# Optimization experiments

Hardware: AMD Instinct MI355X
Metric: run time of the kernel (lower is better)

## Reference

```python
import jax, jax.numpy as jnp
import numpy as np

H, D = 24, 128
HID = H * D  # 3072
IP_DIM = 2048
B, S_IMG, S_TXT, L_IP = 1, 1024, 512, 16
EPS = 1e-6
IP_SCALE = 1.0


def _rms(x, w):
    v = jnp.mean(jnp.square(x), axis=-1, keepdims=True)
    return x * jax.lax.rsqrt(v + EPS) * w


def _heads(x):
    b, s, _ = x.shape
    return x.reshape(b, s, H, D).transpose(0, 2, 1, 3)  # [b,H,s,D]


def _unheads(x):
    b, h, s, d = x.shape
    return x.transpose(0, 2, 1, 3).reshape(b, s, h * d)


def _rope(x, cos, sin):
    # diffusers flux apply_rotary_emb (use_real, unbind_dim=-1): interleaved pairs
    xr = x.reshape(x.shape[:-1] + (D // 2, 2))
    xrot = jnp.stack([-xr[..., 1], xr[..., 0]], axis=-1).reshape(x.shape)
    return x * cos + xrot * sin


def _sdpa(q, k, v):
    scale = 1.0 / jnp.sqrt(jnp.asarray(D, q.dtype))
    s = jnp.einsum('bhqd,bhkd->bhqk', q, k) * scale
    return jnp.einsum('bhqk,bhkd->bhqd', jax.nn.softmax(s, axis=-1), v)


def setup_inputs() -> dict:
    ks = iter(jax.random.split(jax.random.key(0), 24))
    std = 0.02
    lin = lambda k, di, do: std * jax.random.normal(k, (di, do), jnp.float32)
    z = lambda: jnp.zeros((HID,), jnp.float32)
    ones = lambda: jnp.ones((D,), jnp.float32)
    return {
        'hidden_states': jax.random.normal(next(ks), (B, S_IMG, HID), jnp.float32),
        'encoder_hidden_states': jax.random.normal(next(ks), (B, S_TXT, HID), jnp.float32),
        'ip_hidden_states': jax.random.normal(next(ks), (B, L_IP, IP_DIM), jnp.float32),
        'rope_cos': jax.random.uniform(next(ks), (S_TXT + S_IMG, D), jnp.float32),
        'rope_sin': jax.random.uniform(next(ks), (S_TXT + S_IMG, D), jnp.float32),
        'Wq': lin(next(ks), HID, HID), 'bq': z(),
        'Wk': lin(next(ks), HID, HID), 'bk': z(),
        'Wv': lin(next(ks), HID, HID), 'bv': z(),
        'norm_q_w': ones(), 'norm_k_w': ones(),
        'Waq': lin(next(ks), HID, HID), 'baq': z(),
        'Wak': lin(next(ks), HID, HID), 'bak': z(),
        'Wav': lin(next(ks), HID, HID), 'bav': z(),
        'norm_added_q_w': ones(), 'norm_added_k_w': ones(),
        'Wo': lin(next(ks), HID, HID), 'bo': z(),
        'Wadd_out': lin(next(ks), HID, HID), 'badd_out': z(),
        'Wk_ip': lin(next(ks), IP_DIM, HID), 'bk_ip': z(),
        'Wv_ip': lin(next(ks), IP_DIM, HID), 'bv_ip': z(),
        'norm_ip_q_w': ones(), 'norm_ip_k_w': ones(),
    }


def reference(hidden_states, encoder_hidden_states, ip_hidden_states, rope_cos, rope_sin,
              Wq, bq, Wk, bk, Wv, bv, norm_q_w, norm_k_w,
              Waq, baq, Wak, bak, Wav, bav, norm_added_q_w, norm_added_k_w,
              Wo, bo, Wadd_out, badd_out,
              Wk_ip, bk_ip, Wv_ip, bv_ip, norm_ip_q_w, norm_ip_k_w):
    s_txt = encoder_hidden_states.shape[1]
    # image-token projections
    q = hidden_states @ Wq + bq
    k = hidden_states @ Wk + bk
    v = hidden_states @ Wv + bv

    # IP-adapter cross-attention branch (uses q pre-RMSNorm / pre-RoPE)
    ip_q = _rms(_heads(q), norm_ip_q_w)                               # [B,H,S_img,D]
    ip_k = _rms(_heads(ip_hidden_states @ Wk_ip + bk_ip), norm_ip_k_w)  # [B,H,L_ip,D]
    ip_v = _heads(ip_hidden_states @ Wv_ip + bv_ip)
    ip_out = _unheads(_sdpa(ip_q, ip_k, ip_v))                        # [B,S_img,HID]

    qh = _rms(_heads(q), norm_q_w)
    kh = _rms(_heads(k), norm_k_w)
    vh = _heads(v)

    # text-token (encoder) projections
    eq = _rms(_heads(encoder_hidden_states @ Waq + baq), norm_added_q_w)
    ek = _rms(_heads(encoder_hidden_states @ Wak + bak), norm_added_k_w)
    ev = _heads(encoder_hidden_states @ Wav + bav)

    qf = _rope(jnp.concatenate([eq, qh], axis=2), rope_cos, rope_sin)
    kf = _rope(jnp.concatenate([ek, kh], axis=2), rope_cos, rope_sin)
    vf = jnp.concatenate([ev, vh], axis=2)

    out = _unheads(_sdpa(qf, kf, vf))                                 # [B,S_txt+S_img,HID]
    enc_out, img_out = out[:, :s_txt], out[:, s_txt:]
    img_out = img_out + ip_out * IP_SCALE
    img_out = img_out @ Wo + bo
    enc_out = enc_out @ Wadd_out + badd_out
    return (img_out, enc_out)
```

## Files before the change

kernel.cpp:

```cpp
#include <hip/hip_runtime.h>

typedef __bf16 bf16x8 __attribute__((ext_vector_type(8)));
typedef float f32x4 __attribute__((ext_vector_type(4)));
typedef unsigned short u16;
typedef unsigned int u32;

#define QSCALE 0.08838834764831845f

static __device__ __forceinline__ float bf2f(u16 u) {
  union { float f; u32 i; } x; x.i = ((u32)u) << 16; return x.f;
}
static __device__ __forceinline__ u16 f2bf(float f) {
  union { float f; u32 i; } x; x.f = f;
  u32 r = x.i + 0x7fffu + ((x.i >> 16) & 1u);
  return (u16)(r >> 16);
}
static __device__ __forceinline__ void gload16(const void* gp, void* lp) {
  __builtin_amdgcn_global_load_lds(
      (const __attribute__((address_space(1))) u32*)gp,
      (__attribute__((address_space(3))) u32*)lp, 16, 0, 0);
}

__global__ __launch_bounds__(256) void k_conv_acts(
    const float* __restrict__ hs, const float* __restrict__ ehs, const float* __restrict__ iph,
    u16* __restrict__ hsb, u16* __restrict__ ehsb, u16* __restrict__ ipb)
{
  int i = blockIdx.x * 256 + threadIdx.x;
  const float* s; u16* d; int j;
  if (i < 786432)        { s = hs;  d = hsb;  j = i; }
  else if (i < 1179648)  { s = ehs; d = ehsb; j = i - 786432; }
  else                   { s = iph; d = ipb;  j = i - 1179648; }
  float4 v = ((const float4*)s)[j];
  uint2 o;
  o.x = (u32)f2bf(v.x) | ((u32)f2bf(v.y) << 16);
  o.y = (u32)f2bf(v.z) | ((u32)f2bf(v.w) << 16);
  ((uint2*)d)[j] = o;
}

struct WT { const float* src; u16* dst; int K; };
struct WTPack { WT w[10]; };

__global__ __launch_bounds__(256) void k_transp_w(WTPack p)
{
  WT d = p.w[blockIdx.z];
  int K = d.K;
  int k0 = blockIdx.y * 128;
  if (k0 >= K) return;
  int n0 = blockIdx.x * 128;
  __shared__ u32 T[128 * 64];
  int t = threadIdx.x;
  int lane = t & 63, w = t >> 6;
  const float* s = d.src + (size_t)(k0 + w * 32) * 3072 + n0 + lane * 2;
  float2 v[32];
  #pragma unroll
  for (int j = 0; j < 32; j++)
    v[j] = *(const float2*)(s + (size_t)j * 3072);
  int n = lane * 2;
  u32* r0 = T + (size_t)n * 64;
  u32* r1 = r0 + 64;
  int s0 = n & 31, s1 = (n + 1) & 31;
  #pragma unroll
  for (int pp = 0; pp < 16; pp++) {
    int c = w * 16 + pp;
    float2 a = v[2 * pp], b = v[2 * pp + 1];
    r0[c ^ s0] = (u32)f2bf(a.x) | ((u32)f2bf(b.x) << 16);
    r1[c ^ s1] = (u32)f2bf(a.y) | ((u32)f2bf(b.y) << 16);
  }
  __syncthreads();
  #pragma unroll
  for (int i = 0; i < 8; i++) {
    int idx = t + i * 256;
    int row = idx >> 4, ch = idx & 15;
    const u32* r2 = T + (size_t)row * 64;
    int sw = row & 31;
    uint4 o;
    o.x = r2[(ch * 4 + 0) ^ sw];
    o.y = r2[(ch * 4 + 1) ^ sw];
    o.z = r2[(ch * 4 + 2) ^ sw];
    o.w = r2[(ch * 4 + 3) ^ sw];
    *(uint4*)(d.dst + (size_t)(n0 + row) * K + k0 + ch * 8) = o;
  }
}

struct G8Job { const u16* A; const u16* W; const float* bias; void* C; int M; int K; int blk0; int out_f32; };
struct G8Pack { G8Job j[8]; int njobs; };

__global__ __launch_bounds__(512, 2) void k_gemm8(G8Pack p)
{
  extern __shared__ __align__(16) u16 smem[];
  u16* As = smem;
  u16* Bs = smem + 32768;

  int bid = blockIdx.x;
  bid = (bid & 7) * 30 + (bid >> 3);
  int ji = 0;
  while (ji + 1 < p.njobs && bid >= p.j[ji + 1].blk0) ji++;
  G8Job J = p.j[ji];
  int local = bid - J.blk0;
  int m0 = (local / 12) * 256;
  int n0 = (local % 12) * 256;
  int K = J.K, NT = K >> 6;

  int tid = threadIdx.x, w = tid >> 6, lane = tid & 63, l15 = lane & 15, quad = lane >> 4;
  int wm = (w >> 2) * 128, wn = (w & 3) * 64;
  int dw = w * 512;
  int cread = (quad ^ (l15 & 3)) * 8;

  int rr = tid >> 2;
  int c4 = ((tid & 3) ^ (rr & 3)) * 8;
  const u16* pa0 = J.A + (size_t)(m0 + rr) * K + c4;
  const u16* pa1 = pa0 + (size_t)128 * K;
  const u16* pb0 = J.W + (size_t)(n0 + rr) * K + c4;
  const u16* pb1 = pb0 + (size_t)128 * K;

  f32x4 acc[8][4] = {};
  bf16x8 af[4], bfr[4];

#define STAGE_A(b, kh, tt) do { int _ko = (tt) * 64 + (kh) * 32; int _d = ((b) * 2 + (kh)) * 8192 + dw; \
    gload16(pa0 + _ko, As + _d); gload16(pa1 + _ko, As + _d + 4096); } while (0)
#define STAGE_B(b, kh, tt) do { int _ko = (tt) * 64 + (kh) * 32; int _d = ((b) * 2 + (kh)) * 8192 + dw; \
    gload16(pb0 + _ko, Bs + _d); gload16(pb1 + _ko, Bs + _d + 4096); } while (0)

  STAGE_A(0, 0, 0); STAGE_B(0, 0, 0); STAGE_A(0, 1, 0); STAGE_B(0, 1, 0);
  STAGE_A(1, 0, 1); STAGE_B(1, 0, 1);
  __asm__ volatile("s_waitcnt vmcnt(4)" ::: "memory");
  __builtin_amdgcn_s_barrier();

#define PHASE(ks, mtb, READB, STAGES, WAITS) do { \
    int _ab = (cur * 2 + (ks)) * 8192; \
    _Pragma("unroll") for (int i = 0; i < 4; i++) \
      af[i] = *(const bf16x8*)(As + _ab + (wm + ((mtb) + i) * 16 + l15) * 32 + cread); \
    if (READB) { _Pragma("unroll") for (int i = 0; i < 4; i++) \
      bfr[i] = *(const bf16x8*)(Bs + _ab + (wn + i * 16 + l15) * 32 + cread); } \
    STAGES; WAITS; \
    __builtin_amdgcn_s_barrier(); \
    __asm__ volatile("s_waitcnt lgkmcnt(0)" ::: "memory"); \
    __builtin_amdgcn_sched_barrier(0); \
    __builtin_amdgcn_s_setprio(1); \
    _Pragma("unroll") for (int mt = 0; mt < 4; mt++) \
      _Pragma("unroll") for (int nt = 0; nt < 4; nt++) \
        acc[(mtb) + mt][nt] = __builtin_amdgcn_mfma_f32_16x16x32_bf16(af[mt], bfr[nt], acc[(mtb) + mt][nt], 0, 0, 0); \
    __builtin_amdgcn_s_setprio(0); \
    __builtin_amdgcn_sched_barrier(0); \
    __builtin_amdgcn_s_barrier(); \
  } while (0)

  int cur = 0;
  for (int t = 0; t < NT; t++) {
    int o = cur ^ 1;
    int t1 = (t + 1 < NT) ? t + 1 : NT - 1;
    int t2 = (t + 2 < NT) ? t + 2 : NT - 1;
    PHASE(0, 0, 1, STAGE_A(o, 1, t1), (void)0);
    PHASE(0, 4, 0, STAGE_B(o, 1, t1), __asm__ volatile("s_waitcnt vmcnt(8)" ::: "memory"));
    PHASE(1, 0, 1, STAGE_A(cur, 0, t2), (void)0);
    PHASE(1, 4, 0, STAGE_B(cur, 0, t2), __asm__ volatile("s_waitcnt vmcnt(8)" ::: "memory"));
    cur = o;
  }
  __asm__ volatile("s_waitcnt vmcnt(0)" ::: "memory");

  #pragma unroll
  for (int mt = 0; mt < 8; mt++) {
    int row = m0 + wm + mt * 16 + quad * 4;
    #pragma unroll
    for (int nt = 0; nt < 4; nt++) {
      int col = n0 + wn + nt * 16 + l15;
      float bv = J.bias[col];
      #pragma unroll
      for (int r = 0; r < 4; r++) {
        if (row + r < J.M) {
          float v = acc[mt][nt][r] + bv;
          if (J.out_f32) ((float*)J.C)[(size_t)(row + r) * 3072 + col] = v;
          else           ((u16*)J.C)[(size_t)(row + r) * 3072 + col] = f2bf(v);
        }
      }
    }
  }
#undef PHASE
#undef STAGE_A
#undef STAGE_B
}

struct GJob { const u16* A; const u16* W; const float* bias; void* C; int M; int K; int blk0; int out_f32; };
struct GPack { GJob j[8]; int njobs; };

template<int MT>
__global__ __launch_bounds__(256) void k_gemm(GPack p)
{
  __shared__ u16 As[MT * 64];
  __shared__ u16 Bs[128 * 64];
  int bid = blockIdx.x;
  int ji = 0;
  while (ji + 1 < p.njobs && bid >= p.j[ji+1].blk0) ji++;
  GJob J = p.j[ji];
  int local = bid - J.blk0;
  int m0 = (local / 24) * MT;
  int n0 = (local % 24) * 128;

  int tid = threadIdx.x, w = tid >> 6, lane = tid & 63, l15 = lane & 15, quad = lane >> 4;
  constexpr int MF = MT / 32;
  int wm = (w >> 1) * (MT / 2), wn = (w & 1) * 64;
  f32x4 acc[MF][4] = {};

  constexpr int GA = MT * 8 / 256;
  const u16* Ag[GA]; const u16* Bg[4];
  #pragma unroll
  for (int i = 0; i < GA; i++) {
    int s = i * 256 + tid;
    int row = s >> 3, kc = (s & 7) ^ (row & 7);
    Ag[i] = J.A + (size_t)(m0 + row) * J.K + kc * 8;
  }
  #pragma unroll
  for (int i = 0; i < 4; i++) {
    int s = i * 256 + tid;
    int row = s >> 3, kc = (s & 7) ^ (row & 7);
    Bg[i] = J.W + (size_t)(n0 + row) * J.K + kc * 8;
  }

  for (int k0 = 0; k0 < J.K; k0 += 64) {
    #pragma unroll
    for (int i = 0; i < GA; i++)
      gload16(Ag[i] + k0, As + (size_t)(i * 256 + w * 64) * 8);
    #pragma unroll
    for (int i = 0; i < 4; i++)
      gload16(Bg[i] + k0, Bs + (size_t)(i * 256 + w * 64) * 8);
    __syncthreads();
    int x7 = l15 & 7;
    #pragma unroll
    for (int ks = 0; ks < 2; ks++) {
      bf16x8 af[MF], bfr[4];
      #pragma unroll
      for (int t = 0; t < MF; t++)
        af[t] = *(const bf16x8*)(As + (wm + t * 16 + l15) * 64 + (((ks * 4 + quad) ^ x7) * 8));
      #pragma unroll
      for (int t = 0; t < 4; t++)
        bfr[t] = *(const bf16x8*)(Bs + (wn + t * 16 + l15) * 64 + (((ks * 4 + quad) ^ x7) * 8));
      #pragma unroll
      for (int mt = 0; mt < MF; mt++)
        #pragma unroll
        for (int nt = 0; nt < 4; nt++)
          acc[mt][nt] = __builtin_amdgcn_mfma_f32_16x16x32_bf16(af[mt], bfr[nt], acc[mt][nt], 0, 0, 0);
    }
    __syncthreads();
  }

  #pragma unroll
  for (int mt = 0; mt < MF; mt++) {
    int row = m0 + wm + mt * 16 + quad * 4;
    #pragma unroll
    for (int nt = 0; nt < 4; nt++) {
      int col = n0 + wn + nt * 16 + l15;
      float bv = J.bias[col];
      #pragma unroll
      for (int r = 0; r < 4; r++) {
        if (row + r < J.M) {
          float v = acc[mt][nt][r] + bv;
          if (J.out_f32) ((float*)J.C)[(size_t)(row + r) * 3072 + col] = v;
          else           ((u16*)J.C)[(size_t)(row + r) * 3072 + col] = f2bf(v);
        }
      }
    }
  }
}

__global__ __launch_bounds__(256) void k_pack_qk(
    const u16* __restrict__ q, const u16* __restrict__ k,
    const u16* __restrict__ eq, const u16* __restrict__ ek,
    const u16* __restrict__ ipk,
    const float* __restrict__ cosr, const float* __restrict__ sinr,
    const float* __restrict__ nq, const float* __restrict__ nk,
    const float* __restrict__ naq, const float* __restrict__ nak,
    const float* __restrict__ nipq, const float* __restrict__ nipk,
    u16* __restrict__ Qf, u16* __restrict__ Kf, u16* __restrict__ Qip, u16* __restrict__ Kip)
{
  int u = blockIdx.x * 4 + (threadIdx.x >> 6);
  int lane = threadIdx.x & 63;
  int d0 = lane * 2;
  if (u < 36864) {
    int t = u / 24, h = u % 24;
    bool txt = t < 512;
    const u16* qrow = txt ? eq + (size_t)t * 3072 : q + (size_t)(t - 512) * 3072;
    const u16* krow = txt ? ek + (size_t)t * 3072 : k + (size_t)(t - 512) * 3072;
    u32 qv = ((const u32*)(qrow + h * 128))[lane];
    u32 kv = ((const u32*)(krow + h * 128))[lane];
    float q0 = bf2f((u16)qv), q1 = bf2f((u16)(qv >> 16));
    float k0 = bf2f((u16)kv), k1 = bf2f((u16)(kv >> 16));
    float sq = q0 * q0 + q1 * q1, sk = k0 * k0 + k1 * k1;
    #pragma unroll
    for (int off = 32; off > 0; off >>= 1) {
      sq += __shfl_xor(sq, off, 64);
      sk += __shfl_xor(sk, off, 64);
    }
    float rq = rsqrtf(sq * (1.0f / 128.0f) + 1e-6f);
    float rk = rsqrtf(sk * (1.0f / 128.0f) + 1e-6f);
    const float* wq = txt ? naq : nq;
    const float* wk = txt ? nak : nk;
    float2 c = ((const float2*)(cosr + (size_t)t * 128))[lane];
    float2 s = ((const float2*)(sinr + (size_t)t * 128))[lane];
    float xq0 = q0 * rq * wq[d0] * QSCALE, xq1 = q1 * rq * wq[d0 + 1] * QSCALE;
    float xk0 = k0 * rk * wk[d0],          xk1 = k1 * rk * wk[d0 + 1];
    u32 oq = (u32)f2bf(xq0 * c.x - xq1 * s.x) | ((u32)f2bf(xq1 * c.y + xq0 * s.y) << 16);
    u32 ok = (u32)f2bf(xk0 * c.x - xk1 * s.x) | ((u32)f2bf(xk1 * c.y + xk0 * s.y) << 16);
    ((u32*)(Qf + ((size_t)h * 1536 + t) * 128))[lane] = oq;
    ((u32*)(Kf + ((size_t)h * 1536 + t) * 128))[lane] = ok;
    if (!txt) {
      float y0 = q0 * rq * nipq[d0] * QSCALE, y1 = q1 * rq * nipq[d0 + 1] * QSCALE;
      u32 oy = (u32)f2bf(y0) | ((u32)f2bf(y1) << 16);
      ((u32*)(Qip + ((size_t)h * 1024 + (t - 512)) * 128))[lane] = oy;
    }
  } else {
    int u2 = u - 36864;
    if (u2 < 384) {
      int h = u2 >> 4, t = u2 & 15;
      u32 v = ((const u32*)(ipk + (size_t)t * 3072 + h * 128))[lane];
      float x0 = bf2f((u16)v), x1 = bf2f((u16)(v >> 16));
      float ss = x0 * x0 + x1 * x1;
      #pragma unroll
      for (int off = 32; off > 0; off >>= 1) ss += __shfl_xor(ss, off, 64);
      float rr = rsqrtf(ss * (1.0f / 128.0f) + 1e-6f);
      u32 o = (u32)f2bf(x0 * rr * nipk[d0]) | ((u32)f2bf(x1 * rr * nipk[d0 + 1]) << 16);
      ((u32*)(Kip + ((size_t)h * 64 + t) * 128))[lane] = o;
    }
  }
}

__global__ __launch_bounds__(256) void k_pack_v(
    const u16* __restrict__ v, const u16* __restrict__ ev, const u16* __restrict__ ipv,
    u16* __restrict__ Vt, u16* __restrict__ Vipt)
{
  __shared__ u16 T[64 * 72];
  int h = blockIdx.x, y = blockIdx.y, tid = threadIdx.x;
  if (y < 48) {
    int tb = (y % 24) * 64, db = (y / 24) * 64;
    #pragma unroll
    for (int i = 0; i < 2; i++) {
      int idx = tid + i * 256;
      int r = idx >> 3, ch = idx & 7;
      int t = tb + r;
      const u16* src = (t < 512) ? ev + (size_t)t * 3072 : v + (size_t)(t - 512) * 3072;
      uint4 val = *(const uint4*)(src + h * 128 + db + ch * 8);
      u16 tmp[8];
      *(uint4*)tmp = val;
      #pragma unroll
      for (int j = 0; j < 8; j++) T[(ch * 8 + j) * 72 + r] = tmp[j];
    }
    __syncthreads();
    #pragma unroll
    for (int i = 0; i < 2; i++) {
      int idx = tid + i * 256;
      int r = idx >> 3, ch = idx & 7;
      uint4 val = *(const uint4*)(T + r * 72 + ch * 8);
      *(uint4*)(Vt + ((size_t)h * 128 + db + r) * 1536 + tb + ch * 8) = val;
    }
  } else {
    if (tid < 128) {
      #pragma unroll
      for (int t = 0; t < 64; t++) {
        u16 val = 0;
        if (t < 16) val = ipv[(size_t)t * 3072 + h * 128 + tid];
        Vipt[((size_t)h * 128 + tid) * 64 + t] = val;
      }
    }
  }
}

__global__ __launch_bounds__(256) void k_attn(
    const u16* __restrict__ Q, const u16* __restrict__ K, const u16* __restrict__ V,
    const float* __restrict__ addend, void* __restrict__ out,
    int Sq, int Skv, int Skv_valid, int mode)
{
  __shared__ u16 Ks[64 * 128];
  __shared__ u16 Vs[128 * 64];
  __shared__ u16 Ps[4 * 16 * 68];
  int tid = threadIdx.x, h = blockIdx.y;
  int w = tid >> 6, lane = tid & 63, l15 = lane & 15, quad = lane >> 4;
  int mb = blockIdx.x * 64 + w * 16;

  bf16x8 aq[4];
  {
    const u16* qp = Q + ((size_t)h * Sq + mb + l15) * 128 + quad * 8;
    #pragma unroll
    for (int c = 0; c < 4; c++) aq[c] = *(const bf16x8*)(qp + c * 32);
  }

  const u16* Kg[4]; const u16* Vg[4];
  #pragma unroll
  for (int i = 0; i < 4; i++) {
    int s = tid + i * 256;
    int key = s >> 4, kc = (s & 15) ^ (key & 15);
    Kg[i] = K + ((size_t)h * Skv + key) * 128 + kc * 8;
    int d = s >> 3, vc = (s & 7) ^ (d & 7);
    Vg[i] = V + ((size_t)h * 128 + d) * Skv + vc * 8;
  }

  f32x4 o[8] = {};
  float m_col = -3.0e38f, l_col = 0.0f;
  u16* myPs = Ps + w * (16 * 68);

  for (int kb = 0; kb < Skv; kb += 64) {
    #pragma unroll
    for (int i = 0; i < 4; i++) {
      gload16(Kg[i] + (size_t)kb * 128, Ks + (i * 256 + w * 64) * 8);
      gload16(Vg[i] + kb,               Vs + (i * 256 + w * 64) * 8);
    }
    __syncthreads();

    f32x4 sc[4];
    #pragma unroll
    for (int mt = 0; mt < 4; mt++) {
      f32x4 a = {0.f, 0.f, 0.f, 0.f};
      int key = mt * 16 + l15;
      #pragma unroll
      for (int c = 0; c < 4; c++) {
        bf16x8 kf = *(const bf16x8*)(Ks + key * 128 + (((c * 4 + quad) ^ l15) * 8));
        a = __builtin_amdgcn_mfma_f32_16x16x32_bf16(kf, aq[c], a, 0, 0, 0);
      }
      sc[mt] = a;
    }
    if (Skv_valid != Skv) {
      #pragma unroll
      for (int mt = 0; mt < 4; mt++)
        #pragma unroll
        for (int r = 0; r < 4; r++)
          if (kb + mt * 16 + quad * 4 + r >= Skv_valid) sc[mt][r] = -1e30f;
    }

    float mx = sc[0][0];
    #pragma unroll
    for (int mt = 0; mt < 4; mt++)
      #pragma unroll
      for (int r = 0; r < 4; r++) mx = fmaxf(mx, sc[mt][r]);
    mx = fmaxf(mx, __shfl_xor(mx, 16, 64));
    mx = fmaxf(mx, __shfl_xor(mx, 32, 64));
    float mn = fmaxf(m_col, mx);
    float alpha = __expf(m_col - mn);
    m_col = mn;

    float sum = 0.f;
    #pragma unroll
    for (int mt = 0; mt < 4; mt++) {
      u16 pk[4];
      #pragma unroll
      for (int r = 0; r < 4; r++) {
        float pp = __expf(sc[mt][r] - mn);
        sum += pp;
        pk[r] = f2bf(pp);
      }
      uint2 pv;
      pv.x = (u32)pk[0] | ((u32)pk[1] << 16);
      pv.y = (u32)pk[2] | ((u32)pk[3] << 16);
      *(uint2*)(myPs + l15 * 68 + mt * 16 + quad * 4) = pv;
    }
    sum += __shfl_xor(sum, 16, 64);
    sum += __shfl_xor(sum, 32, 64);
    l_col = l_col * alpha + sum;

    float ar[4];
    #pragma unroll
    for (int r = 0; r < 4; r++) ar[r] = __shfl(alpha, quad * 4 + r, 64);
    #pragma unroll
    for (int nt = 0; nt < 8; nt++) {
      o[nt][0] *= ar[0]; o[nt][1] *= ar[1]; o[nt][2] *= ar[2]; o[nt][3] *= ar[3];
    }

    __asm__ volatile("s_waitcnt lgkmcnt(0)" ::: "memory");
    #pragma unroll
    for (int kc = 0; kc < 2; kc++) {
      bf16x8 pa = *(const bf16x8*)(myPs + l15 * 68 + kc * 32 + quad * 8);
      #pragma unroll
      for (int nt = 0; nt < 8; nt++) {
        int d = nt * 16 + l15;
        bf16x8 vf = *(const bf16x8*)(Vs + d * 64 + (((kc * 4 + quad) ^ (d & 7)) * 8));
        o[nt] = __builtin_amdgcn_mfma_f32_16x16x32_bf16(pa, vf, o[nt], 0, 0, 0);
      }
    }
    __syncthreads();
  }

  float linv = 1.0f / l_col;
  float lr[4];
  #pragma unroll
  for (int r = 0; r < 4; r++) lr[r] = __shfl(linv, quad * 4 + r, 64);
  #pragma unroll
  for (int r = 0; r < 4; r++) {
    int t = mb + quad * 4 + r;
    size_t base = (size_t)t * 3072 + h * 128 + l15;
    if (mode == 0) {
      float* O = (float*)out;
      #pragma unroll
      for (int nt = 0; nt < 8; nt++) O[base + nt * 16] = o[nt][r] * lr[r];
    } else {
      u16* O = (u16*)out;
      #pragma unroll
      for (int nt = 0; nt < 8; nt++) {
        float vv = o[nt][r] * lr[r];
        if (t >= 512) vv += addend[(size_t)(t - 512) * 3072 + h * 128 + nt * 16 + l15];
        O[base + nt * 16] = f2bf(vv);
      }
    }
  }
}

extern "C" void kernel_launch(void* const* d_in, const int* in_sizes, int n_in,
                              void* d_out, int out_size, void* d_ws, size_t ws_size,
                              hipStream_t stream) {
  const float* hs   = (const float*)d_in[0];
  const float* ehs  = (const float*)d_in[1];
  const float* iph  = (const float*)d_in[2];
  const float* cosr = (const float*)d_in[3];
  const float* sinr = (const float*)d_in[4];
  const float* Wq   = (const float*)d_in[5];  const float* bq   = (const float*)d_in[6];
  const float* Wk   = (const float*)d_in[7];  const float* bk   = (const float*)d_in[8];
  const float* Wv   = (const float*)d_in[9];  const float* bv   = (const float*)d_in[10];
  const float* nq   = (const float*)d_in[11]; const float* nk   = (const float*)d_in[12];
  const float* Waq  = (const float*)d_in[13]; const float* baq  = (const float*)d_in[14];
  const float* Wak  = (const float*)d_in[15]; const float* bak  = (const float*)d_in[16];
  const float* Wav  = (const float*)d_in[17]; const float* bav  = (const float*)d_in[18];
  const float* naq  = (const float*)d_in[19]; const float* nak  = (const float*)d_in[20];
  const float* Wo   = (const float*)d_in[21]; const float* bo   = (const float*)d_in[22];
  const float* Wad  = (const float*)d_in[23]; const float* bad  = (const float*)d_in[24];
  const float* Wkip = (const float*)d_in[25]; const float* bkip = (const float*)d_in[26];
  const float* Wvip = (const float*)d_in[27]; const float* bvip = (const float*)d_in[28];
  const float* nipq = (const float*)d_in[29]; const float* nipk = (const float*)d_in[30];
  (void)in_sizes; (void)n_in; (void)out_size; (void)ws_size;

  char* ws = (char*)d_ws;
  size_t off = 0;
  auto alloc = [&](size_t bytes) { size_t o = off; off += (bytes + 255) & ~(size_t)255; return o; };

  u16* hsb  = (u16*)(ws + alloc((size_t)1024 * 3072 * 2));
  u16* ehsb = (u16*)(ws + alloc((size_t)512 * 3072 * 2));
  u16* ipb  = (u16*)(ws + alloc((size_t)16 * 2048 * 2));
  u16* WT_[10];
  for (int i = 0; i < 10; i++) WT_[i] = (u16*)(ws + alloc((size_t)3072 * (i < 8 ? 3072 : 2048) * 2));
  u16* qb   = (u16*)(ws + alloc((size_t)1024 * 3072 * 2));
  u16* kb_  = (u16*)(ws + alloc((size_t)1024 * 3072 * 2));
  u16* vb   = (u16*)(ws + alloc((size_t)1024 * 3072 * 2));
  u16* eqb  = (u16*)(ws + alloc((size_t)512 * 3072 * 2));
  u16* ekb  = (u16*)(ws + alloc((size_t)512 * 3072 * 2));
  u16* evb  = (u16*)(ws + alloc((size_t)512 * 3072 * 2));
  u16* ipkb = (u16*)(ws + alloc((size_t)16 * 3072 * 2));
  u16* ipvb = (u16*)(ws + alloc((size_t)16 * 3072 * 2));
  u16* Qf   = (u16*)(ws + alloc((size_t)24 * 1536 * 128 * 2));
  u16* Kff  = (u16*)(ws + alloc((size_t)24 * 1536 * 128 * 2));
  u16* Vt   = (u16*)(ws + alloc((size_t)24 * 128 * 1536 * 2));
  u16* Qip  = (u16*)(ws + alloc((size_t)24 * 1024 * 128 * 2));
  u16* Kip  = (u16*)(ws + alloc((size_t)24 * 64 * 128 * 2));
  u16* Vipt = (u16*)(ws + alloc((size_t)24 * 128 * 64 * 2));
  float* ip_out = (float*)(ws + alloc((size_t)1024 * 3072 * 4));
  u16* attnb = (u16*)(ws + alloc((size_t)1536 * 3072 * 2));

  static bool attr_done = false;
  if (!attr_done) {
    hipFuncSetAttribute((const void*)k_gemm8, hipFuncAttributeMaxDynamicSharedMemorySize, 131072);
    attr_done = true;
  }

  k_conv_acts<<<4640, 256, 0, stream>>>(hs, ehs, iph, hsb, ehsb, ipb);

  WTPack p;
  const float* wsrc[10] = {Wq, Wk, Wv, Waq, Wak, Wav, Wo, Wad, Wkip, Wvip};
  for (int i = 0; i < 10; i++) { p.w[i].src = wsrc[i]; p.w[i].dst = WT_[i]; p.w[i].K = (i < 8 ? 3072 : 2048); }
  k_transp_w<<<dim3(24, 24, 10), 256, 0, stream>>>(p);

  {
    G8Pack pp;
    const u16* As_[8]  = {hsb, hsb, hsb, ehsb, ehsb, ehsb, ipb, ipb};
    const u16* Ws_[8]  = {WT_[0], WT_[1], WT_[2], WT_[3], WT_[4], WT_[5], WT_[8], WT_[9]};
    const float* bs_[8] = {bq, bk, bv, baq, bak, bav, bkip, bvip};
    u16* Cs_[8]        = {qb, kb_, vb, eqb, ekb, evb, ipkb, ipvb};
    int Ms_[8] = {1024, 1024, 1024, 512, 512, 512, 16, 16};
    int Ks_[8] = {3072, 3072, 3072, 3072, 3072, 3072, 2048, 2048};
    int blk = 0;
    for (int i = 0; i < 8; i++) {
      pp.j[i].A = As_[i]; pp.j[i].W = Ws_[i]; pp.j[i].bias = bs_[i]; pp.j[i].C = Cs_[i];
      pp.j[i].M = Ms_[i]; pp.j[i].K = Ks_[i]; pp.j[i].blk0 = blk; pp.j[i].out_f32 = 0;
      blk += ((Ms_[i] + 255) / 256) * 12;
    }
    pp.njobs = 8;
    k_gemm8<<<dim3(blk), 512, 131072, stream>>>(pp);
  }

  k_pack_qk<<<9312, 256, 0, stream>>>(qb, kb_, eqb, ekb, ipkb, cosr, sinr, nq, nk, naq, nak, nipq, nipk, Qf, Kff, Qip, Kip);
  k_pack_v<<<dim3(24, 49), 256, 0, stream>>>(vb, evb, ipvb, Vt, Vipt);

  k_attn<<<dim3(16, 24), 256, 0, stream>>>(Qip, Kip, Vipt, (const float*)nullptr, ip_out, 1024, 64, 16, 0);
  k_attn<<<dim3(24, 24), 256, 0, stream>>>(Qf, Kff, Vt, ip_out, attnb, 1536, 1536, 1536, 1);

  {
    GPack pp;
    float* out = (float*)d_out;
    pp.j[0].A = attnb + (size_t)512 * 3072; pp.j[0].W = WT_[6]; pp.j[0].bias = bo;
    pp.j[0].C = out; pp.j[0].M = 1024; pp.j[0].K = 3072; pp.j[0].blk0 = 0; pp.j[0].out_f32 = 1;
    pp.j[1].A = attnb; pp.j[1].W = WT_[7]; pp.j[1].bias = bad;
    pp.j[1].C = out + (size_t)1024 * 3072; pp.j[1].M = 512; pp.j[1].K = 3072;
    pp.j[1].blk0 = (1024 / 64) * 24; pp.j[1].out_f32 = 1;
    pp.njobs = 2;
    k_gemm<64><<<dim3((1024 / 64) * 24 + (512 / 64) * 24), 256, 0, stream>>>(pp);
  }
}
```

Measured before the change: 676.7 us.

## Fuse fp32 weight load and bf16 conversion into projection GEMM, drop pre-transpose

The QKV/added/IP projection GEMM now reads the fp32 weight matrices directly from global memory into registers, converts them to bf16 and writes them transposed into shared memory. This replaces the separate transpose-and-convert pass for eight of the ten weights. That pass wrote bf16 copies of the weights, which the GEMM then read back. The main loop is reorganised around the register-staged B loads. The trade-off is that B tiles move as twice as many fp32 bytes and need more registers for staging. Weight traffic is also re-read once per M-tile instead of once overall, which may cost more than the removed pass for multi-tile jobs.

Result: faster. 663.0 us (-2.0%).

```diff
diff --git a/kernel.cpp b/kernel.cpp
--- a/kernel.cpp
+++ b/kernel.cpp
@@ -14,6 +14,9 @@
   union { float f; u32 i; } x; x.f = f;
   u32 r = x.i + 0x7fffu + ((x.i >> 16) & 1u);
   return (u16)(r >> 16);
+}
+static __device__ __forceinline__ u16 bfc(float f) {
+  union { __bf16 b; u16 u; } c; c.b = (__bf16)f; return c.u;
 }
 static __device__ __forceinline__ void gload16(const void* gp, void* lp) {
   __builtin_amdgcn_global_load_lds(
@@ -38,7 +41,7 @@
 }
 
 struct WT { const float* src; u16* dst; int K; };
-struct WTPack { WT w[10]; };
+struct WTPack { WT w[2]; };
 
 __global__ __launch_bounds__(256) void k_transp_w(WTPack p)
 {
@@ -82,7 +85,7 @@
   }
 }
 
-struct G8Job { const u16* A; const u16* W; const float* bias; void* C; int M; int K; int blk0; int out_f32; };
+struct G8Job { const u16* A; const float* Wf; const float* bias; void* C; int M; int K; int blk0; int out_f32; };
 struct G8Pack { G8Job j[8]; int njobs; };
 
 __global__ __launch_bounds__(512, 2) void k_gemm8(G8Pack p)
@@ -110,29 +113,35 @@
   int c4 = ((tid & 3) ^ (rr & 3)) * 8;
   const u16* pa0 = J.A + (size_t)(m0 + rr) * K + c4;
   const u16* pa1 = pa0 + (size_t)128 * K;
-  const u16* pb0 = J.W + (size_t)(n0 + rr) * K + c4;
-  const u16* pb1 = pb0 + (size_t)128 * K;
-
+
+  int nB = (tid & 127) * 2;
+  int kcB = tid >> 7;
+  int khB = kcB >> 1;
+  const float* pw = J.Wf + (size_t)(kcB * 16) * 3072 + n0 + nB;
+
+  float2 ld[16];
   f32x4 acc[8][4] = {};
   bf16x8 af[4], bfr[4];
 
-#define STAGE_A(b, kh, tt) do { int _ko = (tt) * 64 + (kh) * 32; int _d = ((b) * 2 + (kh)) * 8192 + dw; \
+#define A_GLOAD(b, kh, tt) do { size_t _ko = (size_t)(tt) * 64 + (kh) * 32; int _d = ((b) * 2 + (kh)) * 8192 + dw; \
     gload16(pa0 + _ko, As + _d); gload16(pa1 + _ko, As + _d + 4096); } while (0)
-#define STAGE_B(b, kh, tt) do { int _ko = (tt) * 64 + (kh) * 32; int _d = ((b) * 2 + (kh)) * 8192 + dw; \
-    gload16(pb0 + _ko, Bs + _d); gload16(pb1 + _ko, Bs + _d + 4096); } while (0)
-
-  STAGE_A(0, 0, 0); STAGE_B(0, 0, 0); STAGE_A(0, 1, 0); STAGE_B(0, 1, 0);
-  STAGE_A(1, 0, 1); STAGE_B(1, 0, 1);
-  __asm__ volatile("s_waitcnt vmcnt(4)" ::: "memory");
-  __builtin_amdgcn_s_barrier();
-
-#define PHASE(ks, mtb, READB, STAGES, WAITS) do { \
-    int _ab = (cur * 2 + (ks)) * 8192; \
+#define B_ISSUE(tt) do { const float* _s = pw + (size_t)(tt) * 64 * 3072; \
+    _Pragma("unroll") for (int j = 0; j < 16; j++) ld[j] = *(const float2*)(_s + (size_t)j * 3072); } while (0)
+#define B_WRITE(b) do { \
+    _Pragma("unroll") for (int j2 = 0; j2 < 2; j2++) { \
+      int _c = 2 * (kcB & 1) + j2; \
+      u16 t0[8], t1[8]; \
+      _Pragma("unroll") for (int i = 0; i < 8; i++) { float2 _v = ld[j2 * 8 + i]; t0[i] = bfc(_v.x); t1[i] = bfc(_v.y); } \
+      *(uint4*)(Bs + ((b) * 2 + khB) * 8192 + nB * 32 + ((_c ^ (nB & 3))) * 8) = *(uint4*)t0; \
+      *(uint4*)(Bs + ((b) * 2 + khB) * 8192 + (nB + 1) * 32 + ((_c ^ ((nB + 1) & 3))) * 8) = *(uint4*)t1; \
+    } } while (0)
+#define FRAGS_A(mtb, ks) do { int _ab = (cur * 2 + (ks)) * 8192; \
     _Pragma("unroll") for (int i = 0; i < 4; i++) \
-      af[i] = *(const bf16x8*)(As + _ab + (wm + ((mtb) + i) * 16 + l15) * 32 + cread); \
-    if (READB) { _Pragma("unroll") for (int i = 0; i < 4; i++) \
-      bfr[i] = *(const bf16x8*)(Bs + _ab + (wn + i * 16 + l15) * 32 + cread); } \
-    STAGES; WAITS; \
+      af[i] = *(const bf16x8*)(As + _ab + (wm + ((mtb) + i) * 16 + l15) * 32 + cread); } while (0)
+#define FRAGS_B(ks) do { int _ab = (cur * 2 + (ks)) * 8192; \
+    _Pragma("unroll") for (int i = 0; i < 4; i++) \
+      bfr[i] = *(const bf16x8*)(Bs + _ab + (wn + i * 16 + l15) * 32 + cread); } while (0)
+#define MFMA16(mtb) do { \
     __builtin_amdgcn_s_barrier(); \
     __asm__ volatile("s_waitcnt lgkmcnt(0)" ::: "memory"); \
     __builtin_amdgcn_sched_barrier(0); \
@@ -145,15 +154,35 @@
     __builtin_amdgcn_s_barrier(); \
   } while (0)
 
+  B_ISSUE(0);
+  A_GLOAD(0, 0, 0);
+  A_GLOAD(0, 1, 0);
+  B_WRITE(0);
+  B_ISSUE(1);
+  A_GLOAD(1, 0, 1);
+  __asm__ volatile("s_waitcnt vmcnt(18)" ::: "memory");
+  __asm__ volatile("s_waitcnt lgkmcnt(0)" ::: "memory");
+  __builtin_amdgcn_s_barrier();
+
   int cur = 0;
   for (int t = 0; t < NT; t++) {
     int o = cur ^ 1;
-    int t1 = (t + 1 < NT) ? t + 1 : NT - 1;
-    int t2 = (t + 2 < NT) ? t + 2 : NT - 1;
-    PHASE(0, 0, 1, STAGE_A(o, 1, t1), (void)0);
-    PHASE(0, 4, 0, STAGE_B(o, 1, t1), __asm__ volatile("s_waitcnt vmcnt(8)" ::: "memory"));
-    PHASE(1, 0, 1, STAGE_A(cur, 0, t2), (void)0);
-    PHASE(1, 4, 0, STAGE_B(cur, 0, t2), __asm__ volatile("s_waitcnt vmcnt(8)" ::: "memory"));
+    int t1c = (t + 1 < NT) ? t + 1 : NT - 1;
+    int t2c = (t + 2 < NT) ? t + 2 : NT - 1;
+    FRAGS_A(0, 0); FRAGS_B(0);
+    A_GLOAD(o, 1, t1c);
+    MFMA16(0);
+    FRAGS_A(4, 0);
+    MFMA16(4);
+    __asm__ volatile("s_waitcnt vmcnt(20)" ::: "memory");
+    FRAGS_A(0, 1); FRAGS_B(1);
+    B_WRITE(o);
+    B_ISSUE(t2c);
+    A_GLOAD(cur, 0, t2c);
+    MFMA16(0);
+    FRAGS_A(4, 1);
+    __asm__ volatile("s_waitcnt vmcnt(18)" ::: "memory");
+    MFMA16(4);
     cur = o;
   }
   __asm__ volatile("s_waitcnt vmcnt(0)" ::: "memory");
@@ -175,9 +204,12 @@
       }
     }
   }
-#undef PHASE
-#undef STAGE_A
-#undef STAGE_B
+#undef MFMA16
+#undef FRAGS_B
+#undef FRAGS_A
+#undef B_WRITE
+#undef B_ISSUE
+#undef A_GLOAD
 }
 
 struct GJob { const u16* A; const u16* W; const float* bias; void* C; int M; int K; int blk0; int out_f32; };
@@ -530,8 +562,8 @@
   u16* hsb  = (u16*)(ws + alloc((size_t)1024 * 3072 * 2));
   u16* ehsb = (u16*)(ws + alloc((size_t)512 * 3072 * 2));
   u16* ipb  = (u16*)(ws + alloc((size_t)16 * 2048 * 2));
-  u16* WT_[10];
-  for (int i = 0; i < 10; i++) WT_[i] = (u16*)(ws + alloc((size_t)3072 * (i < 8 ? 3072 : 2048) * 2));
+  u16* WT_[2];
+  for (int i = 0; i < 2; i++) WT_[i] = (u16*)(ws + alloc((size_t)3072 * 3072 * 2));
   u16* qb   = (u16*)(ws + alloc((size_t)1024 * 3072 * 2));
   u16* kb_  = (u16*)(ws + alloc((size_t)1024 * 3072 * 2));
   u16* vb   = (u16*)(ws + alloc((size_t)1024 * 3072 * 2));
@@ -558,21 +590,21 @@
   k_conv_acts<<<4640, 256, 0, stream>>>(hs, ehs, iph, hsb, ehsb, ipb);
 
   WTPack p;
-  const float* wsrc[10] = {Wq, Wk, Wv, Waq, Wak, Wav, Wo, Wad, Wkip, Wvip};
-  for (int i = 0; i < 10; i++) { p.w[i].src = wsrc[i]; p.w[i].dst = WT_[i]; p.w[i].K = (i < 8 ? 3072 : 2048); }
-  k_transp_w<<<dim3(24, 24, 10), 256, 0, stream>>>(p);
+  p.w[0].src = Wo;  p.w[0].dst = WT_[0]; p.w[0].K = 3072;
+  p.w[1].src = Wad; p.w[1].dst = WT_[1]; p.w[1].K = 3072;
+  k_transp_w<<<dim3(24, 24, 2), 256, 0, stream>>>(p);
 
   {
     G8Pack pp;
-    const u16* As_[8]  = {hsb, hsb, hsb, ehsb, ehsb, ehsb, ipb, ipb};
-    const u16* Ws_[8]  = {WT_[0], WT_[1], WT_[2], WT_[3], WT_[4], WT_[5], WT_[8], WT_[9]};
-    const float* bs_[8] = {bq, bk, bv, baq, bak, bav, bkip, bvip};
-    u16* Cs_[8]        = {qb, kb_, vb, eqb, ekb, evb, ipkb, ipvb};
+    const u16* As_[8]    = {hsb, hsb, hsb, ehsb, ehsb, ehsb, ipb, ipb};
+    const float* Ws_[8]  = {Wq, Wk, Wv, Waq, Wak, Wav, Wkip, Wvip};
+    const float* bs_[8]  = {bq, bk, bv, baq, bak, bav, bkip, bvip};
+    u16* Cs_[8]          = {qb, kb_, vb, eqb, ekb, evb, ipkb, ipvb};
     int Ms_[8] = {1024, 1024, 1024, 512, 512, 512, 16, 16};
     int Ks_[8] = {3072, 3072, 3072, 3072, 3072, 3072, 2048, 2048};
     int blk = 0;
     for (int i = 0; i < 8; i++) {
-      pp.j[i].A = As_[i]; pp.j[i].W = Ws_[i]; pp.j[i].bias = bs_[i]; pp.j[i].C = Cs_[i];
+      pp.j[i].A = As_[i]; pp.j[i].Wf = Ws_[i]; pp.j[i].bias = bs_[i]; pp.j[i].C = Cs_[i];
       pp.j[i].M = Ms_[i]; pp.j[i].K = Ks_[i]; pp.j[i].blk0 = blk; pp.j[i].out_f32 = 0;
       blk += ((Ms_[i] + 255) / 256) * 12;
     }
@@ -589,9 +621,9 @@
   {
     GPack pp;
     float* out = (float*)d_out;
-    pp.j[0].A = attnb + (size_t)512 * 3072; pp.j[0].W = WT_[6]; pp.j[0].bias = bo;
+    pp.j[0].A = attnb + (size_t)512 * 3072; pp.j[0].W = WT_[0]; pp.j[0].bias = bo;
     pp.j[0].C = out; pp.j[0].M = 1024; pp.j[0].K = 3072; pp.j[0].blk0 = 0; pp.j[0].out_f32 = 1;
-    pp.j[1].A = attnb; pp.j[1].W = WT_[7]; pp.j[1].bias = bad;
+    pp.j[1].A = attnb; pp.j[1].W = WT_[1]; pp.j[1].bias = bad;
     pp.j[1].C = out + (size_t)1024 * 3072; pp.j[1].M = 512; pp.j[1].K = 3072;
     pp.j[1].blk0 = (1024 / 64) * 24; pp.j[1].out_f32 = 1;
     pp.njobs = 2;
```
